# Kernel tuning notes

Hardware: AMD Instinct MI355X
Metric: run time of the kernel (lower is better)

The kernel has to match this reference:

```python
import jax, jax.numpy as jnp
import numpy as np

B, T, F, H = 512, 1024, 64, 64  # batch, seq_len, n_feats, hidden


def setup_inputs() -> dict:
    key = jax.random.key(0)
    ks = jax.random.split(key, 12)
    s = 1.0 / np.sqrt(H)  # torch LSTM init scale: U(-1/sqrt(H), 1/sqrt(H))
    u = lambda k, shape: jax.random.uniform(k, shape, jnp.float32, -s, s)
    return {
        "x": jax.random.normal(ks[0], (B, T, F), jnp.float32),
        "w_ih0": u(ks[1], (4 * H, F)),
        "w_hh0": u(ks[2], (4 * H, H)),
        "b_ih0": u(ks[3], (4 * H,)),
        "b_hh0": u(ks[4], (4 * H,)),
        "w_ih1": u(ks[5], (4 * H, H)),
        "w_hh1": u(ks[6], (4 * H, H)),
        "b_ih1": u(ks[7], (4 * H,)),
        "b_hh1": u(ks[8], (4 * H,)),
        "fc_w": u(ks[9], (1, H)),
        "fc_b": u(ks[10], (1,)),
    }


def _lstm_layer(x, w_ih, w_hh, b_ih, b_hh):
    """Single LSTM layer, torch gate order (i, f, g, o). x: [B, T, in] -> [B, T, H]."""
    bsz = x.shape[0]
    h_dim = w_hh.shape[1]
    # Precompute all input projections in one big GEMM: [B, T, 4H]
    pre = jnp.einsum("bti,gi->btg", x, w_ih) + b_ih + b_hh

    def step(carry, p_t):
        h, c = carry
        z = p_t + h @ w_hh.T  # [B, 4H]
        i, f, g, o = jnp.split(z, 4, axis=-1)
        c = jax.nn.sigmoid(f) * c + jax.nn.sigmoid(i) * jnp.tanh(g)
        h = jax.nn.sigmoid(o) * jnp.tanh(c)
        return (h, c), h

    h0 = jnp.zeros((bsz, h_dim), x.dtype)
    (_, _), hs = jax.lax.scan(step, (h0, h0), jnp.swapaxes(pre, 0, 1))  # hs: [T, B, H]
    return jnp.swapaxes(hs, 0, 1)


def reference(x, w_ih0, w_hh0, b_ih0, b_hh0, w_ih1, w_hh1, b_ih1, b_hh1, fc_w, fc_b):
    h1 = _lstm_layer(x, w_ih0, w_hh0, b_ih0, b_hh0)   # [B, T, H]
    # (inter-layer dropout p=0.2 is train-only in torch; eval-mode reference omits it)
    h2 = _lstm_layer(h1, w_ih1, w_hh1, b_ih1, b_hh1)  # [B, T, H]
    return h2[:, -1] @ fc_w.T + fc_b                  # [B, 1]
```

## Files before the change

kernel.cpp:

```cpp
#include <hip/hip_runtime.h>
#include <hip/hip_bf16.h>


typedef _Float16 f16x8 __attribute__((ext_vector_type(8)));
typedef float f32x4  __attribute__((ext_vector_type(4)));

#define MFMAH(A, B, C) __builtin_amdgcn_mfma_f32_16x16x32_f16(A, B, C, 0, 0, 0)

constexpr int T_LEN = 1024;
constexpr int H     = 64;
constexpr int NCH   = 8;
constexpr int NTHR  = 1024;
constexpr int NBLK  = 64;

constexpr int    XT_HALFS   = 2 * 4 * 8 * 8;
constexpr size_t XBLK_HALFS = (size_t)T_LEN * XT_HALFS;

__device__ __forceinline__ float sigm_f(float x) {
  return __builtin_amdgcn_rcpf(1.0f + __expf(-x));
}
__device__ __forceinline__ float tanh_f(float x) {
  return 1.0f - 2.0f * __builtin_amdgcn_rcpf(1.0f + __expf(2.0f * x));
}
__device__ __forceinline__ unsigned dpp_xor1_u32(unsigned v) {
  return (unsigned)__builtin_amdgcn_mov_dpp((int)v, 0xB1, 0xF, 0xF, true);
}

__global__ __launch_bounds__(256, 4) void xconv(const float* __restrict__ x,
                                                _Float16* __restrict__ xf) {
  const int gid = blockIdx.x * 256 + threadIdx.x;
  const int lq    = gid & 3;
  const int t     = (gid >> 2) & (T_LEN - 1);
  const int chain = gid >> 12;
  const int ch  = chain & 7;
  const int blk = chain >> 3;
  const float* src = x + ((size_t)chain * T_LEN + t) * H + 8 * lq;
  float4 v0 = *reinterpret_cast<const float4*>(src);
  float4 v1 = *reinterpret_cast<const float4*>(src + 4);
  float4 v2 = *reinterpret_cast<const float4*>(src + 32);
  float4 v3 = *reinterpret_cast<const float4*>(src + 36);
  float a[8]  = {v0.x, v0.y, v0.z, v0.w, v1.x, v1.y, v1.z, v1.w};
  float c8[8] = {v2.x, v2.y, v2.z, v2.w, v3.x, v3.y, v3.z, v3.w};
  f16x8 p0, p1;
#pragma unroll
  for (int e = 0; e < 8; ++e) {
    p0[e] = (_Float16)a[e];
    p1[e] = (_Float16)c8[e];
  }
  _Float16* dst = xf + (size_t)blk * XBLK_HALFS + (size_t)t * XT_HALFS +
                  lq * 64 + ch * 8;
  *reinterpret_cast<f16x8*>(dst)       = p0;
  *reinterpret_cast<f16x8*>(dst + 256) = p1;
}

__global__ __launch_bounds__(NTHR) void lstm_fused(
    const _Float16* __restrict__ xf,
    const float* __restrict__ w_ih0, const float* __restrict__ w_hh0,
    const float* __restrict__ b_ih0, const float* __restrict__ b_hh0,
    const float* __restrict__ w_ih1, const float* __restrict__ w_hh1,
    const float* __restrict__ b_ih1, const float* __restrict__ b_hh1,
    const float* __restrict__ fc_w, const float* __restrict__ fc_b,
    float* __restrict__ out) {
  const int tid = threadIdx.x;
  const int wv  = tid >> 6;
  const int L   = wv >> 3;
  const int w8  = wv & 7;
  const int l   = tid & 63;
  const int col = l & 15;
  const int lq  = l >> 4;
  const int blk = blockIdx.x;

  __shared__ __align__(16) _Float16 hb[2][2][512];
  __shared__ __align__(16) float zp[2][8][260];
  __shared__ float bias_s[2][256];
  __shared__ float fcw_s[H];
  __shared__ float hfin[NCH][H];

  for (int i = tid; i < 2 * 2 * 512; i += NTHR) ((_Float16*)hb)[i] = (_Float16)0.f;
  if (tid < 256)       bias_s[0][tid] = b_ih0[tid] + b_hh0[tid];
  else if (tid < 512)  bias_s[1][tid - 256] = b_ih1[tid - 256] + b_hh1[tid - 256];
  if (tid < H) fcw_s[tid] = fc_w[tid];

  const float* wih = L ? w_ih1 : w_ih0;
  const float* whh = L ? w_hh1 : w_hh0;
  f16x8 w16[2][4];
#pragma unroll
  for (int rt = 0; rt < 2; ++rt) {
#pragma unroll
    for (int kt = 0; kt < 4; ++kt) {
      const int row = 32 * w8 + 16 * rt + col;
      const int k0  = 32 * kt + 8 * lq;
      const float* src = (k0 < 64) ? &wih[row * 64 + k0] : &whh[row * 64 + (k0 - 64)];
      float4 v0 = *reinterpret_cast<const float4*>(src);
      float4 v1 = *reinterpret_cast<const float4*>(src + 4);
      float vv[8] = {v0.x, v0.y, v0.z, v0.w, v1.x, v1.y, v1.z, v1.w};
      f16x8 h8;
#pragma unroll
      for (int e = 0; e < 8; ++e) h8[e] = (_Float16)vv[e];
      w16[rt][kt] = h8;
    }
  }

  __syncthreads();

  const int rdoff = lq * 64 + (col & 7) * 8;
  const int gch = l >> 3;
  const int gf  = w8 * 8 + (l & 7);
  const int hword = w8 * 32 + (l >> 1);
  float cst = 0.0f;

  const _Float16* xfl = xf + (size_t)blk * XBLK_HALFS + rdoff;
  f16x8 xb0, xb1, xbn0, xbn1;
  if (L == 0) {
    xb0 = *reinterpret_cast<const f16x8*>(xfl);
    xb1 = *reinterpret_cast<const f16x8*>(xfl + 256);
  }

  const f32x4 zf4 = {0.f, 0.f, 0.f, 0.f};

#define ZSTORE(Lidx)                                                       \
  if (col < 8) {                                                           \
    *reinterpret_cast<f32x4*>(&zp[Lidx][col][32 * w8 + 4 * lq])      = a0; \
    *reinterpret_cast<f32x4*>(&zp[Lidx][col][32 * w8 + 16 + 4 * lq]) = a1; \
  }

#define GATES(Lidx, hv_)                                            \
  {                                                                 \
    const float* zrow = &zp[Lidx][gch][0];                          \
    float z0 = zrow[gf]       + bias_s[Lidx][gf];                   \
    float z1 = zrow[64 + gf]  + bias_s[Lidx][64 + gf];              \
    float z2 = zrow[128 + gf] + bias_s[Lidx][128 + gf];             \
    float z3 = zrow[192 + gf] + bias_s[Lidx][192 + gf];             \
    float ig = sigm_f(z0), fg = sigm_f(z1);                         \
    float gg = tanh_f(z2), og = sigm_f(z3);                         \
    cst = fg * cst + ig * gg;                                       \
    hv_ = og * tanh_f(cst);                                         \
  }

#define HSTORE(base_, hv_)                                          \
  {                                                                 \
    _Float16 hf = (_Float16)(hv_);                                  \
    unsigned me = (unsigned)__builtin_bit_cast(unsigned short, hf); \
    unsigned nb = dpp_xor1_u32(me);                                 \
    if ((l & 1) == 0)                                               \
      reinterpret_cast<unsigned*>(base_)[hword] = me | (nb << 16);  \
  }

  for (int t = 0; t <= T_LEN + 1; ++t) {
    if (L == 0) {
      if (t + 1 < T_LEN) {
        const _Float16* p = xfl + (size_t)(t + 1) * XT_HALFS;
        xbn0 = *reinterpret_cast<const f16x8*>(p);
        xbn1 = *reinterpret_cast<const f16x8*>(p + 256);
      }
      if (t < T_LEN) {
        const _Float16* h0c = &hb[0][(t + 1) & 1][0];
        f16x8 B2 = *reinterpret_cast<const f16x8*>(h0c + rdoff);
        f16x8 B3 = *reinterpret_cast<const f16x8*>(h0c + 256 + rdoff);
        f32x4 a0 = zf4, a1 = zf4;
        a0 = MFMAH(w16[0][0], xb0, a0); a1 = MFMAH(w16[1][0], xb0, a1);
        a0 = MFMAH(w16[0][1], xb1, a0); a1 = MFMAH(w16[1][1], xb1, a1);
        a0 = MFMAH(w16[0][2], B2,  a0); a1 = MFMAH(w16[1][2], B2,  a1);
        a0 = MFMAH(w16[0][3], B3,  a0); a1 = MFMAH(w16[1][3], B3,  a1);
        ZSTORE(0)
      }
    } else {
      if (t >= 2) {
        float hv;
        GATES(1, hv)
        if (t == T_LEN + 1) {
          hfin[gch][gf] = hv;
        } else {
          HSTORE(&hb[1][t & 1][0], hv)
        }
      }
    }

    __syncthreads();

    if (L == 0) {
      if (t < T_LEN) {
        float hv;
        GATES(0, hv)
        HSTORE(&hb[0][t & 1][0], hv)
      }
    } else {
      if (t >= 1 && t <= T_LEN) {
        const _Float16* h0c = &hb[0][(t + 1) & 1][0];
        const _Float16* h1c = &hb[1][t & 1][0];
        f16x8 B0 = *reinterpret_cast<const f16x8*>(h0c + rdoff);
        f16x8 B1 = *reinterpret_cast<const f16x8*>(h0c + 256 + rdoff);
        f16x8 B2 = *reinterpret_cast<const f16x8*>(h1c + rdoff);
        f16x8 B3 = *reinterpret_cast<const f16x8*>(h1c + 256 + rdoff);
        f32x4 a0 = zf4, a1 = zf4;
        a0 = MFMAH(w16[0][0], B0, a0); a1 = MFMAH(w16[1][0], B0, a1);
        a0 = MFMAH(w16[0][1], B1, a0); a1 = MFMAH(w16[1][1], B1, a1);
        a0 = MFMAH(w16[0][2], B2, a0); a1 = MFMAH(w16[1][2], B2, a1);
        a0 = MFMAH(w16[0][3], B3, a0); a1 = MFMAH(w16[1][3], B3, a1);
        ZSTORE(1)
      }
    }

    __syncthreads();
    if (L == 0) { xb0 = xbn0; xb1 = xbn1; }
  }
#undef ZSTORE
#undef GATES
#undef HSTORE

  if (tid < NCH) {
    float acc = fc_b[0];
#pragma unroll
    for (int h = 0; h < H; ++h) acc += fcw_s[h] * hfin[tid][h];
    out[blk * NCH + tid] = acc;
  }
}

extern "C" void kernel_launch(void* const* d_in, const int* in_sizes, int n_in,
                              void* d_out, int out_size, void* d_ws, size_t ws_size,
                              hipStream_t stream) {
  const float* x     = (const float*)d_in[0];
  const float* w_ih0 = (const float*)d_in[1];
  const float* w_hh0 = (const float*)d_in[2];
  const float* b_ih0 = (const float*)d_in[3];
  const float* b_hh0 = (const float*)d_in[4];
  const float* w_ih1 = (const float*)d_in[5];
  const float* w_hh1 = (const float*)d_in[6];
  const float* b_ih1 = (const float*)d_in[7];
  const float* b_hh1 = (const float*)d_in[8];
  const float* fc_w  = (const float*)d_in[9];
  const float* fc_b  = (const float*)d_in[10];
  float* out = (float*)d_out;

  _Float16* xfrag = (_Float16*)d_ws;

  xconv<<<dim3(8192), dim3(256), 0, stream>>>(x, xfrag);
  lstm_fused<<<dim3(NBLK), dim3(NTHR), 0, stream>>>(
      xfrag, w_ih0, w_hh0, b_ih0, b_hh0, w_ih1, w_hh1, b_ih1, b_hh1,
      fc_w, fc_b, out);
}
```

Measured before the change: 824.9 us.

## Compute all four gates per wave in registers, drop the z staging buffer

Each wave now owns 16 hidden features across all four gates (i, f, g, o), so the gate nonlinearities and cell update run directly on the MFMA accumulators instead of being staged through a shared-memory z buffer. This halves the block to 512 threads (4 waves per layer), folds the bias into the accumulator initialisation, and cuts the per-timestep barriers from two to one by pipelining layer 1 one step behind layer 0. The cost is twice as many MFMAs per wave and more weight registers, while the zp round-trip and one barrier per step go away.

```diff
diff --git a/kernel.cpp b/kernel.cpp
--- a/kernel.cpp
+++ b/kernel.cpp
@@ -3,6 +3,7 @@
 
 
 typedef _Float16 f16x8 __attribute__((ext_vector_type(8)));
+typedef _Float16 f16x4 __attribute__((ext_vector_type(4)));
 typedef float f32x4  __attribute__((ext_vector_type(4)));
 
 #define MFMAH(A, B, C) __builtin_amdgcn_mfma_f32_16x16x32_f16(A, B, C, 0, 0, 0)
@@ -10,7 +11,7 @@
 constexpr int T_LEN = 1024;
 constexpr int H     = 64;
 constexpr int NCH   = 8;
-constexpr int NTHR  = 1024;
+constexpr int NTHR  = 512;
 constexpr int NBLK  = 64;
 
 constexpr int    XT_HALFS   = 2 * 4 * 8 * 8;
@@ -21,9 +22,6 @@
 }
 __device__ __forceinline__ float tanh_f(float x) {
   return 1.0f - 2.0f * __builtin_amdgcn_rcpf(1.0f + __expf(2.0f * x));
-}
-__device__ __forceinline__ unsigned dpp_xor1_u32(unsigned v) {
-  return (unsigned)__builtin_amdgcn_mov_dpp((int)v, 0xB1, 0xF, 0xF, true);
 }
 
 __global__ __launch_bounds__(256, 4) void xconv(const float* __restrict__ x,
@@ -53,7 +51,7 @@
   *reinterpret_cast<f16x8*>(dst + 256) = p1;
 }
 
-__global__ __launch_bounds__(NTHR) void lstm_fused(
+__global__ __launch_bounds__(NTHR, 2) void lstm_fused(
     const _Float16* __restrict__ xf,
     const float* __restrict__ w_ih0, const float* __restrict__ w_hh0,
     const float* __restrict__ b_ih0, const float* __restrict__ b_hh0,
@@ -63,32 +61,31 @@
     float* __restrict__ out) {
   const int tid = threadIdx.x;
   const int wv  = tid >> 6;
-  const int L   = wv >> 3;
-  const int w8  = wv & 7;
+  const int L   = wv >> 2;
+  const int w   = wv & 3;
   const int l   = tid & 63;
   const int col = l & 15;
   const int lq  = l >> 4;
   const int blk = blockIdx.x;
 
   __shared__ __align__(16) _Float16 hb[2][2][512];
-  __shared__ __align__(16) float zp[2][8][260];
-  __shared__ float bias_s[2][256];
   __shared__ float fcw_s[H];
   __shared__ float hfin[NCH][H];
 
   for (int i = tid; i < 2 * 2 * 512; i += NTHR) ((_Float16*)hb)[i] = (_Float16)0.f;
-  if (tid < 256)       bias_s[0][tid] = b_ih0[tid] + b_hh0[tid];
-  else if (tid < 512)  bias_s[1][tid - 256] = b_ih1[tid - 256] + b_hh1[tid - 256];
   if (tid < H) fcw_s[tid] = fc_w[tid];
 
   const float* wih = L ? w_ih1 : w_ih0;
   const float* whh = L ? w_hh1 : w_hh0;
-  f16x8 w16[2][4];
-#pragma unroll
-  for (int rt = 0; rt < 2; ++rt) {
+  const float* bih = L ? b_ih1 : b_ih0;
+  const float* bhh = L ? b_hh1 : b_hh0;
+  f16x8 w16[4][4];
+  f32x4 biasf[4];
+#pragma unroll
+  for (int g = 0; g < 4; ++g) {
 #pragma unroll
     for (int kt = 0; kt < 4; ++kt) {
-      const int row = 32 * w8 + 16 * rt + col;
+      const int row = 64 * g + 16 * w + col;
       const int k0  = 32 * kt + 8 * lq;
       const float* src = (k0 < 64) ? &wih[row * 64 + k0] : &whh[row * 64 + (k0 - 64)];
       float4 v0 = *reinterpret_cast<const float4*>(src);
@@ -97,17 +94,22 @@
       f16x8 h8;
 #pragma unroll
       for (int e = 0; e < 8; ++e) h8[e] = (_Float16)vv[e];
-      w16[rt][kt] = h8;
+      w16[g][kt] = h8;
+    }
+#pragma unroll
+    for (int r = 0; r < 4; ++r) {
+      int row = 64 * g + 16 * w + 4 * lq + r;
+      biasf[g][r] = bih[row] + bhh[row];
     }
   }
 
   __syncthreads();
 
   const int rdoff = lq * 64 + (col & 7) * 8;
-  const int gch = l >> 3;
-  const int gf  = w8 * 8 + (l & 7);
-  const int hword = w8 * 32 + (l >> 1);
-  float cst = 0.0f;
+  const int waddr = (w >> 1) * 256 + (2 * (w & 1) + (lq >> 1)) * 64 +
+                    (col & 7) * 8 + 4 * (lq & 1);
+  const int feat0 = 16 * w + 4 * lq;
+  const bool wr_ok = (col < 8);
 
   const _Float16* xfl = xf + (size_t)blk * XBLK_HALFS + rdoff;
   f16x8 xb0, xb1, xbn0, xbn1;
@@ -116,97 +118,68 @@
     xb1 = *reinterpret_cast<const f16x8*>(xfl + 256);
   }
 
-  const f32x4 zf4 = {0.f, 0.f, 0.f, 0.f};
-
-#define ZSTORE(Lidx)                                                       \
-  if (col < 8) {                                                           \
-    *reinterpret_cast<f32x4*>(&zp[Lidx][col][32 * w8 + 4 * lq])      = a0; \
-    *reinterpret_cast<f32x4*>(&zp[Lidx][col][32 * w8 + 16 + 4 * lq]) = a1; \
-  }
-
-#define GATES(Lidx, hv_)                                            \
-  {                                                                 \
-    const float* zrow = &zp[Lidx][gch][0];                          \
-    float z0 = zrow[gf]       + bias_s[Lidx][gf];                   \
-    float z1 = zrow[64 + gf]  + bias_s[Lidx][64 + gf];              \
-    float z2 = zrow[128 + gf] + bias_s[Lidx][128 + gf];             \
-    float z3 = zrow[192 + gf] + bias_s[Lidx][192 + gf];             \
-    float ig = sigm_f(z0), fg = sigm_f(z1);                         \
-    float gg = tanh_f(z2), og = sigm_f(z3);                         \
-    cst = fg * cst + ig * gg;                                       \
-    hv_ = og * tanh_f(cst);                                         \
-  }
-
-#define HSTORE(base_, hv_)                                          \
-  {                                                                 \
-    _Float16 hf = (_Float16)(hv_);                                  \
-    unsigned me = (unsigned)__builtin_bit_cast(unsigned short, hf); \
-    unsigned nb = dpp_xor1_u32(me);                                 \
-    if ((l & 1) == 0)                                               \
-      reinterpret_cast<unsigned*>(base_)[hword] = me | (nb << 16);  \
-  }
-
-  for (int t = 0; t <= T_LEN + 1; ++t) {
-    if (L == 0) {
-      if (t + 1 < T_LEN) {
-        const _Float16* p = xfl + (size_t)(t + 1) * XT_HALFS;
-        xbn0 = *reinterpret_cast<const f16x8*>(p);
-        xbn1 = *reinterpret_cast<const f16x8*>(p + 256);
+  f32x4 cst = {0.f, 0.f, 0.f, 0.f};
+
+  for (int t = 0; t <= T_LEN; ++t) {
+    const bool act = (L == 0) ? (t < T_LEN) : (t >= 1);
+
+    if (L == 0 && t + 1 < T_LEN) {
+      const _Float16* p = xfl + (size_t)(t + 1) * XT_HALFS;
+      xbn0 = *reinterpret_cast<const f16x8*>(p);
+      xbn1 = *reinterpret_cast<const f16x8*>(p + 256);
+    }
+
+    if (act) {
+      const _Float16* h0c = &hb[0][(t + 1) & 1][0];
+      f16x8 B0, B1, B2, B3;
+      if (L == 0) {
+        B0 = xb0;
+        B1 = xb1;
+        B2 = *reinterpret_cast<const f16x8*>(h0c + rdoff);
+        B3 = *reinterpret_cast<const f16x8*>(h0c + 256 + rdoff);
+      } else {
+        const _Float16* h1c = &hb[1][t & 1][0];
+        B0 = *reinterpret_cast<const f16x8*>(h0c + rdoff);
+        B1 = *reinterpret_cast<const f16x8*>(h0c + 256 + rdoff);
+        B2 = *reinterpret_cast<const f16x8*>(h1c + rdoff);
+        B3 = *reinterpret_cast<const f16x8*>(h1c + 256 + rdoff);
       }
-      if (t < T_LEN) {
-        const _Float16* h0c = &hb[0][(t + 1) & 1][0];
-        f16x8 B2 = *reinterpret_cast<const f16x8*>(h0c + rdoff);
-        f16x8 B3 = *reinterpret_cast<const f16x8*>(h0c + 256 + rdoff);
-        f32x4 a0 = zf4, a1 = zf4;
-        a0 = MFMAH(w16[0][0], xb0, a0); a1 = MFMAH(w16[1][0], xb0, a1);
-        a0 = MFMAH(w16[0][1], xb1, a0); a1 = MFMAH(w16[1][1], xb1, a1);
-        a0 = MFMAH(w16[0][2], B2,  a0); a1 = MFMAH(w16[1][2], B2,  a1);
-        a0 = MFMAH(w16[0][3], B3,  a0); a1 = MFMAH(w16[1][3], B3,  a1);
-        ZSTORE(0)
+
+      f32x4 a0 = biasf[0], a1 = biasf[1], a2 = biasf[2], a3 = biasf[3];
+      a0 = MFMAH(w16[0][0], B0, a0); a1 = MFMAH(w16[1][0], B0, a1);
+      a2 = MFMAH(w16[2][0], B0, a2); a3 = MFMAH(w16[3][0], B0, a3);
+      a0 = MFMAH(w16[0][1], B1, a0); a1 = MFMAH(w16[1][1], B1, a1);
+      a2 = MFMAH(w16[2][1], B1, a2); a3 = MFMAH(w16[3][1], B1, a3);
+      a0 = MFMAH(w16[0][2], B2, a0); a1 = MFMAH(w16[1][2], B2, a1);
+      a2 = MFMAH(w16[2][2], B2, a2); a3 = MFMAH(w16[3][2], B2, a3);
+      a0 = MFMAH(w16[0][3], B3, a0); a1 = MFMAH(w16[1][3], B3, a1);
+      a2 = MFMAH(w16[2][3], B3, a2); a3 = MFMAH(w16[3][3], B3, a3);
+
+      f32x4 hv;
+#pragma unroll
+      for (int r = 0; r < 4; ++r) {
+        float ig = sigm_f(a0[r]);
+        float fg = sigm_f(a1[r]);
+        float gg = tanh_f(a2[r]);
+        float og = sigm_f(a3[r]);
+        cst[r] = fg * cst[r] + ig * gg;
+        hv[r]  = og * tanh_f(cst[r]);
       }
-    } else {
-      if (t >= 2) {
-        float hv;
-        GATES(1, hv)
-        if (t == T_LEN + 1) {
-          hfin[gch][gf] = hv;
-        } else {
-          HSTORE(&hb[1][t & 1][0], hv)
-        }
-      }
-    }
-
-    __syncthreads();
-
-    if (L == 0) {
-      if (t < T_LEN) {
-        float hv;
-        GATES(0, hv)
-        HSTORE(&hb[0][t & 1][0], hv)
-      }
-    } else {
-      if (t >= 1 && t <= T_LEN) {
-        const _Float16* h0c = &hb[0][(t + 1) & 1][0];
-        const _Float16* h1c = &hb[1][t & 1][0];
-        f16x8 B0 = *reinterpret_cast<const f16x8*>(h0c + rdoff);
-        f16x8 B1 = *reinterpret_cast<const f16x8*>(h0c + 256 + rdoff);
-        f16x8 B2 = *reinterpret_cast<const f16x8*>(h1c + rdoff);
-        f16x8 B3 = *reinterpret_cast<const f16x8*>(h1c + 256 + rdoff);
-        f32x4 a0 = zf4, a1 = zf4;
-        a0 = MFMAH(w16[0][0], B0, a0); a1 = MFMAH(w16[1][0], B0, a1);
-        a0 = MFMAH(w16[0][1], B1, a0); a1 = MFMAH(w16[1][1], B1, a1);
-        a0 = MFMAH(w16[0][2], B2, a0); a1 = MFMAH(w16[1][2], B2, a1);
-        a0 = MFMAH(w16[0][3], B3, a0); a1 = MFMAH(w16[1][3], B3, a1);
-        ZSTORE(1)
+
+      if (L == 1 && t == T_LEN) {
+        if (wr_ok) *reinterpret_cast<f32x4*>(&hfin[col][feat0]) = hv;
+      } else if (wr_ok) {
+        f16x4 o4;
+#pragma unroll
+        for (int r = 0; r < 4; ++r) o4[r] = (_Float16)hv[r];
+        _Float16* base = L ? &hb[1][(t + 1) & 1][0] : &hb[0][t & 1][0];
+        *reinterpret_cast<f16x4*>(base + waddr) = o4;
       }
     }
 
     __syncthreads();
     if (L == 0) { xb0 = xbn0; xb1 = xbn1; }
   }
-#undef ZSTORE
-#undef GATES
-#undef HSTORE
 
   if (tid < NCH) {
     float acc = fc_b[0];
```

New measurement: 954.4 us. +15.7%, slower.

## Split batch into 256 blocks of 2 chains and use lightweight LDS barriers

Applied to the files above, without the earlier changes.

Each block now handles 2 sequence chains instead of 8, so 256 workgroups are launched instead of 64 and more CUs work in parallel on the latency-bound recurrence. The input/h-state layouts and read/write offsets are rewritten for the smaller chain count, and only 4 waves compute gates (one per chain per layer). __syncthreads is replaced by an explicit lgkmcnt wait plus s_barrier. The cost is that most MFMA output columns are wasted, since 16-wide tiles now carry only 2 real chains, and each block does the same full weight load.

```diff
diff --git a/kernel.cpp b/kernel.cpp
--- a/kernel.cpp
+++ b/kernel.cpp
@@ -9,11 +9,11 @@
 
 constexpr int T_LEN = 1024;
 constexpr int H     = 64;
-constexpr int NCH   = 8;
+constexpr int NCH   = 2;
 constexpr int NTHR  = 1024;
-constexpr int NBLK  = 64;
-
-constexpr int    XT_HALFS   = 2 * 4 * 8 * 8;
+constexpr int NBLK  = 256;
+
+constexpr int    XT_HALFS   = 2 * 4 * 2 * 8;
 constexpr size_t XBLK_HALFS = (size_t)T_LEN * XT_HALFS;
 
 __device__ __forceinline__ float sigm_f(float x) {
@@ -24,6 +24,11 @@
 }
 __device__ __forceinline__ unsigned dpp_xor1_u32(unsigned v) {
   return (unsigned)__builtin_amdgcn_mov_dpp((int)v, 0xB1, 0xF, 0xF, true);
+}
+__device__ __forceinline__ void lds_barrier() {
+  asm volatile("s_waitcnt lgkmcnt(0)" ::: "memory");
+  __builtin_amdgcn_s_barrier();
+  asm volatile("" ::: "memory");
 }
 
 __global__ __launch_bounds__(256, 4) void xconv(const float* __restrict__ x,
@@ -32,8 +37,8 @@
   const int lq    = gid & 3;
   const int t     = (gid >> 2) & (T_LEN - 1);
   const int chain = gid >> 12;
-  const int ch  = chain & 7;
-  const int blk = chain >> 3;
+  const int ch  = chain & 1;
+  const int blk = chain >> 1;
   const float* src = x + ((size_t)chain * T_LEN + t) * H + 8 * lq;
   float4 v0 = *reinterpret_cast<const float4*>(src);
   float4 v1 = *reinterpret_cast<const float4*>(src + 4);
@@ -48,9 +53,9 @@
     p1[e] = (_Float16)c8[e];
   }
   _Float16* dst = xf + (size_t)blk * XBLK_HALFS + (size_t)t * XT_HALFS +
-                  lq * 64 + ch * 8;
-  *reinterpret_cast<f16x8*>(dst)       = p0;
-  *reinterpret_cast<f16x8*>(dst + 256) = p1;
+                  lq * 16 + ch * 8;
+  *reinterpret_cast<f16x8*>(dst)      = p0;
+  *reinterpret_cast<f16x8*>(dst + 64) = p1;
 }
 
 __global__ __launch_bounds__(NTHR) void lstm_fused(
@@ -70,13 +75,13 @@
   const int lq  = l >> 4;
   const int blk = blockIdx.x;
 
-  __shared__ __align__(16) _Float16 hb[2][2][512];
-  __shared__ __align__(16) float zp[2][8][260];
+  __shared__ __align__(16) _Float16 hb[2][2][128];
+  __shared__ __align__(16) float zp[2][2][260];
   __shared__ float bias_s[2][256];
   __shared__ float fcw_s[H];
   __shared__ float hfin[NCH][H];
 
-  for (int i = tid; i < 2 * 2 * 512; i += NTHR) ((_Float16*)hb)[i] = (_Float16)0.f;
+  for (int i = tid; i < 2 * 2 * 128; i += NTHR) ((_Float16*)hb)[i] = (_Float16)0.f;
   if (tid < 256)       bias_s[0][tid] = b_ih0[tid] + b_hh0[tid];
   else if (tid < 512)  bias_s[1][tid - 256] = b_ih1[tid - 256] + b_hh1[tid - 256];
   if (tid < H) fcw_s[tid] = fc_w[tid];
@@ -101,36 +106,29 @@
     }
   }
 
-  __syncthreads();
-
-  const int rdoff = lq * 64 + (col & 7) * 8;
-  const int gch = l >> 3;
-  const int gf  = w8 * 8 + (l & 7);
-  const int hword = w8 * 32 + (l >> 1);
+  const int rdoff = lq * 16 + (col & 1) * 8;
+  const bool is_gate = (wv < 2) || (wv == 10) || (wv == 11);
+  const int gch = wv & 1;
+  const int gh  = l;
+  const int waddr_h = ((gh >> 5) << 6) + (((gh >> 3) & 3) << 4) + (gch << 3) + (gh & 7);
   float cst = 0.0f;
 
   const _Float16* xfl = xf + (size_t)blk * XBLK_HALFS + rdoff;
   f16x8 xb0, xb1, xbn0, xbn1;
   if (L == 0) {
     xb0 = *reinterpret_cast<const f16x8*>(xfl);
-    xb1 = *reinterpret_cast<const f16x8*>(xfl + 256);
+    xb1 = *reinterpret_cast<const f16x8*>(xfl + 64);
   }
 
   const f32x4 zf4 = {0.f, 0.f, 0.f, 0.f};
-
-#define ZSTORE(Lidx)                                                       \
-  if (col < 8) {                                                           \
-    *reinterpret_cast<f32x4*>(&zp[Lidx][col][32 * w8 + 4 * lq])      = a0; \
-    *reinterpret_cast<f32x4*>(&zp[Lidx][col][32 * w8 + 16 + 4 * lq]) = a1; \
-  }
 
 #define GATES(Lidx, hv_)                                            \
   {                                                                 \
     const float* zrow = &zp[Lidx][gch][0];                          \
-    float z0 = zrow[gf]       + bias_s[Lidx][gf];                   \
-    float z1 = zrow[64 + gf]  + bias_s[Lidx][64 + gf];              \
-    float z2 = zrow[128 + gf] + bias_s[Lidx][128 + gf];             \
-    float z3 = zrow[192 + gf] + bias_s[Lidx][192 + gf];             \
+    float z0 = zrow[gh]       + bias_s[Lidx][gh];                   \
+    float z1 = zrow[64 + gh]  + bias_s[Lidx][64 + gh];              \
+    float z2 = zrow[128 + gh] + bias_s[Lidx][128 + gh];             \
+    float z3 = zrow[192 + gh] + bias_s[Lidx][192 + gh];             \
     float ig = sigm_f(z0), fg = sigm_f(z1);                         \
     float gg = tanh_f(z2), og = sigm_f(z3);                         \
     cst = fg * cst + ig * gg;                                       \
@@ -143,43 +141,48 @@
     unsigned me = (unsigned)__builtin_bit_cast(unsigned short, hf); \
     unsigned nb = dpp_xor1_u32(me);                                 \
     if ((l & 1) == 0)                                               \
-      reinterpret_cast<unsigned*>(base_)[hword] = me | (nb << 16);  \
-  }
+      reinterpret_cast<unsigned*>(base_)[waddr_h >> 1] = me | (nb << 16); \
+  }
+
+  __syncthreads();
 
   for (int t = 0; t <= T_LEN + 1; ++t) {
     if (L == 0) {
       if (t + 1 < T_LEN) {
         const _Float16* p = xfl + (size_t)(t + 1) * XT_HALFS;
         xbn0 = *reinterpret_cast<const f16x8*>(p);
-        xbn1 = *reinterpret_cast<const f16x8*>(p + 256);
+        xbn1 = *reinterpret_cast<const f16x8*>(p + 64);
       }
       if (t < T_LEN) {
         const _Float16* h0c = &hb[0][(t + 1) & 1][0];
         f16x8 B2 = *reinterpret_cast<const f16x8*>(h0c + rdoff);
-        f16x8 B3 = *reinterpret_cast<const f16x8*>(h0c + 256 + rdoff);
+        f16x8 B3 = *reinterpret_cast<const f16x8*>(h0c + 64 + rdoff);
         f32x4 a0 = zf4, a1 = zf4;
         a0 = MFMAH(w16[0][0], xb0, a0); a1 = MFMAH(w16[1][0], xb0, a1);
         a0 = MFMAH(w16[0][1], xb1, a0); a1 = MFMAH(w16[1][1], xb1, a1);
         a0 = MFMAH(w16[0][2], B2,  a0); a1 = MFMAH(w16[1][2], B2,  a1);
         a0 = MFMAH(w16[0][3], B3,  a0); a1 = MFMAH(w16[1][3], B3,  a1);
-        ZSTORE(0)
-      }
-    } else {
+        if (col < NCH) {
+          *reinterpret_cast<f32x4*>(&zp[0][col][32 * w8 + 4 * lq])      = a0;
+          *reinterpret_cast<f32x4*>(&zp[0][col][32 * w8 + 16 + 4 * lq]) = a1;
+        }
+      }
+    } else if (is_gate) {
       if (t >= 2) {
         float hv;
         GATES(1, hv)
         if (t == T_LEN + 1) {
-          hfin[gch][gf] = hv;
+          hfin[gch][gh] = hv;
         } else {
           HSTORE(&hb[1][t & 1][0], hv)
         }
       }
     }
 
-    __syncthreads();
+    lds_barrier();
 
     if (L == 0) {
-      if (t < T_LEN) {
+      if (is_gate && t < T_LEN) {
         float hv;
         GATES(0, hv)
         HSTORE(&hb[0][t & 1][0], hv)
@@ -189,22 +192,24 @@
         const _Float16* h0c = &hb[0][(t + 1) & 1][0];
         const _Float16* h1c = &hb[1][t & 1][0];
         f16x8 B0 = *reinterpret_cast<const f16x8*>(h0c + rdoff);
-        f16x8 B1 = *reinterpret_cast<const f16x8*>(h0c + 256 + rdoff);
+        f16x8 B1 = *reinterpret_cast<const f16x8*>(h0c + 64 + rdoff);
         f16x8 B2 = *reinterpret_cast<const f16x8*>(h1c + rdoff);
-        f16x8 B3 = *reinterpret_cast<const f16x8*>(h1c + 256 + rdoff);
+        f16x8 B3 = *reinterpret_cast<const f16x8*>(h1c + 64 + rdoff);
         f32x4 a0 = zf4, a1 = zf4;
         a0 = MFMAH(w16[0][0], B0, a0); a1 = MFMAH(w16[1][0], B0, a1);
         a0 = MFMAH(w16[0][1], B1, a0); a1 = MFMAH(w16[1][1], B1, a1);
         a0 = MFMAH(w16[0][2], B2, a0); a1 = MFMAH(w16[1][2], B2, a1);
         a0 = MFMAH(w16[0][3], B3, a0); a1 = MFMAH(w16[1][3], B3, a1);
-        ZSTORE(1)
+        if (col < NCH) {
+          *reinterpret_cast<f32x4*>(&zp[1][col][32 * w8 + 4 * lq])      = a0;
+          *reinterpret_cast<f32x4*>(&zp[1][col][32 * w8 + 16 + 4 * lq]) = a1;
+        }
       }
     }
 
-    __syncthreads();
+    lds_barrier();
     if (L == 0) { xb0 = xbn0; xb1 = xbn1; }
   }
-#undef ZSTORE
 #undef GATES
 #undef HSTORE
 
```

Measured after the change: 788.0 us. 4.5% less time.
